# Kernel optimization log

Hardware: AMD Instinct MI355X
Metric: run time of the kernel (lower is better)

The kernel has to match this reference:

```python
import jax, jax.numpy as jnp
import numpy as np

R = 16
ALPHA = 32
SCALING = ALPHA / R  # 2.0


def setup_inputs() -> dict:
    key = jax.random.key(0)
    k1, k2, k3, k4, k5 = jax.random.split(key, 5)
    x = jax.random.normal(k1, (8192, 4096), dtype=jnp.float32)
    W = jax.random.normal(k2, (4096, 4096), dtype=jnp.float32) * 0.02
    b = jax.random.normal(k3, (4096,), dtype=jnp.float32) * 0.02
    A = jax.random.uniform(k4, (R, 4096), dtype=jnp.float32)
    B = jax.random.normal(k5, (4096, R), dtype=jnp.float32) * 0.02
    return {"x": x, "W": W, "b": b, "A": A, "B": B}


def reference(x, W, b, A, B):
    # base linear: x @ W.T + b
    base = jnp.einsum("ni,oi->no", x, W) + b
    # LoRA path, reassociated: scaling * ((x @ A.T) @ B.T)
    # mathematically identical to x @ (scaling * (B @ A)).T but O(r*(in+out)) per token
    lora = SCALING * jnp.einsum("nr,or->no", jnp.einsum("ni,ri->nr", x, A), B)
    return base + lora
```

## Files before the change

kernel.cpp:

```cpp
#include <hip/hip_runtime.h>
#include <stdint.h>

typedef unsigned short u16;
typedef __bf16 bf16x8 __attribute__((ext_vector_type(8)));
typedef u16   u16x8  __attribute__((ext_vector_type(8)));
typedef float f32x4  __attribute__((ext_vector_type(4)));
typedef float f32x16 __attribute__((ext_vector_type(16)));

#define GLOBAL_AS __attribute__((address_space(1)))
#define LDS_AS __attribute__((address_space(3)))

#define MDIM 8192
#define NDIM 4096
#define KDIM 4096
#define RDIM 16

#define BM 128
#define BN 128
#define BK 64
#define EXTS 40

#define XBF_OFF 0
#define WBF_OFF (MDIM * KDIM * 2)
#define ABF_OFF (WBF_OFF + NDIM * KDIM * 2)
#define T_OFF   (ABF_OFF + RDIM * KDIM * 2)
#define WS_NEED ((size_t)T_OFF + MDIM * RDIM * 4)

#define XN8 (MDIM * KDIM / 8)
#define WN8 (NDIM * KDIM / 8)
#define AN8 (RDIM * KDIM / 8)

__device__ __forceinline__ u16 f2bf(float f) {
    union { float f; uint32_t u; } un;
    un.f = f;
    uint32_t u = un.u;
    u += 0x7FFFu + ((u >> 16) & 1u);
    return (u16)(u >> 16);
}

__device__ __forceinline__ void cvt8(const float* __restrict__ p, u16* __restrict__ d) {
    f32x4 a = *(const f32x4*)p;
    f32x4 b = *(const f32x4*)(p + 4);
    u16x8 o;
    o[0] = f2bf(a[0]); o[1] = f2bf(a[1]); o[2] = f2bf(a[2]); o[3] = f2bf(a[3]);
    o[4] = f2bf(b[0]); o[5] = f2bf(b[1]); o[6] = f2bf(b[2]); o[7] = f2bf(b[3]);
    *(u16x8*)d = o;
}

__global__ __launch_bounds__(256) void cvt_all_kernel(
        const float* __restrict__ x, const float* __restrict__ W,
        const float* __restrict__ A,
        u16* __restrict__ xbf, u16* __restrict__ Wbf, u16* __restrict__ Abf) {
    const int total = XN8 + WN8 + AN8;
    int i = blockIdx.x * blockDim.x + threadIdx.x;
    const int stride = gridDim.x * blockDim.x;
    for (; i < total; i += stride) {
        if (i < XN8) {
            cvt8(x + (size_t)i * 8, xbf + (size_t)i * 8);
        } else if (i < XN8 + WN8) {
            const int j = i - XN8;
            cvt8(W + (size_t)j * 8, Wbf + (size_t)j * 8);
        } else {
            const int j = i - XN8 - WN8;
            cvt8(A + (size_t)j * 8, Abf + (size_t)j * 8);
        }
    }
}

__global__ __launch_bounds__(256) void lora_t_kernel(
        const u16* __restrict__ x, const u16* __restrict__ A,
        float* __restrict__ t) {
    const int wave = threadIdx.x >> 6;
    const int lane = threadIdx.x & 63;
    const int rl   = lane & 15;
    const int quad = lane >> 4;
    const int m0   = (blockIdx.x * 4 + wave) * 16;

    const u16* xp = x + (size_t)(m0 + rl) * KDIM + quad * 8;
    const u16* ap = A + (size_t)rl * KDIM + quad * 8;

    f32x4 acc = {0.f, 0.f, 0.f, 0.f};
#pragma unroll 8
    for (int k = 0; k < KDIM; k += 32) {
        bf16x8 av = *(const bf16x8*)(xp + k);
        bf16x8 bv = *(const bf16x8*)(ap + k);
        acc = __builtin_amdgcn_mfma_f32_16x16x32_bf16(av, bv, acc, 0, 0, 0);
    }
    const int orow = m0 + quad * 4;
#pragma unroll
    for (int v = 0; v < 4; ++v)
        t[(size_t)(orow + v) * RDIM + rl] = acc[v];
}

__global__ __launch_bounds__(256) void lora_t_inline_kernel(
        const float* __restrict__ x, const float* __restrict__ A,
        float* __restrict__ t) {
    const int wave = threadIdx.x >> 6;
    const int lane = threadIdx.x & 63;
    const int rl   = lane & 15;
    const int quad = lane >> 4;
    const int m0   = (blockIdx.x * 4 + wave) * 16;

    const float* xp = x + (size_t)(m0 + rl) * KDIM + quad * 8;
    const float* ap = A + (size_t)rl * KDIM + quad * 8;

    f32x4 acc = {0.f, 0.f, 0.f, 0.f};
    for (int k = 0; k < KDIM; k += 32) {
        f32x4 a0 = *(const f32x4*)(xp + k), a1 = *(const f32x4*)(xp + k + 4);
        f32x4 b0 = *(const f32x4*)(ap + k), b1 = *(const f32x4*)(ap + k + 4);
        u16x8 av, bv;
#pragma unroll
        for (int j = 0; j < 4; ++j) {
            av[j] = f2bf(a0[j]); av[j + 4] = f2bf(a1[j]);
            bv[j] = f2bf(b0[j]); bv[j + 4] = f2bf(b1[j]);
        }
        acc = __builtin_amdgcn_mfma_f32_16x16x32_bf16(
            (bf16x8)av, (bf16x8)bv, acc, 0, 0, 0);
    }
    const int orow = m0 + quad * 4;
#pragma unroll
    for (int v = 0; v < 4; ++v)
        t[(size_t)(orow + v) * RDIM + rl] = acc[v];
}

#define BK2   64
#define HTILE 8192
#define ABUF  16384
#define BOFFS 32768
#define NKT   (KDIM / BK2)

#define STAGE(gsrc, half, kt, par, ab) do {                                   \
    const int _b = (par) * ABUF + (ab) * BOFFS + (half) * HTILE;              \
    _Pragma("unroll")                                                         \
    for (int _q = 0; _q < 2; ++_q) {                                          \
        const int _c   = _q * 512 + tid;                                      \
        const int _row = _c >> 3;                                             \
        const int _kc  = (_c & 7) ^ (_row & 7);                               \
        __builtin_amdgcn_global_load_lds(                                     \
            (const GLOBAL_AS uint32_t*)((gsrc) +                              \
                (size_t)((half) * 128 + _row) * KDIM + (kt) * BK2 + _kc * 8), \
            (LDS_AS uint32_t*)(smem + _b + _c * 8), 16, 0, 0);                \
    } } while (0)

#define NOSTAGE ((void)0)
#define VM0 asm volatile("s_waitcnt vmcnt(0)" ::: "memory")

#define READ_A32(dst, ab_, c) do {                                            \
    _Pragma("unroll")                                                         \
    for (int h = 0; h < 2; ++h)                                               \
        _Pragma("unroll")                                                     \
        for (int r = 0; r < 2; ++r) {                                         \
            const int rh = wm * 64 + r * 32 + l31;                            \
            dst[h][r] = *(const bf16x8*)((ab_) + h * HTILE + rh * 64 +        \
                                         ((((c) * 2 + hi) ^ (rh & 7)) * 8));  \
        } } while (0)

#define READ_B32(dst, bb_, c) do {                                            \
    _Pragma("unroll")                                                         \
    for (int cb = 0; cb < 2; ++cb) {                                          \
        const int rh = wn * 32 + l31;                                         \
        dst[cb] = *(const bf16x8*)((bb_) + cb * HTILE + rh * 64 +             \
                                   ((((c) * 2 + hi) ^ (rh & 7)) * 8));        \
    } } while (0)

#define MFMA32(a_, b_) do {                                                   \
    __builtin_amdgcn_s_setprio(1);                                            \
    _Pragma("unroll")                                                         \
    for (int h = 0; h < 2; ++h)                                               \
        _Pragma("unroll")                                                     \
        for (int r = 0; r < 2; ++r)                                           \
            _Pragma("unroll")                                                 \
            for (int cb = 0; cb < 2; ++cb)                                    \
                acc[h][r][cb] = __builtin_amdgcn_mfma_f32_32x32x16_bf16(      \
                    a_[h][r], b_[cb], acc[h][r][cb], 0, 0, 0);                \
    __builtin_amdgcn_s_setprio(0);                                            \
} while (0)

#define BARRIER __builtin_amdgcn_s_barrier()

#define KT32(ab_, bb_, S1, S2, S3, S4, WEND) do {                             \
    READ_A32(aF, ab_, 0); READ_B32(bF, bb_, 0);                               \
    S1; S2;                                                                   \
    READ_A32(aN, ab_, 1); READ_B32(bN, bb_, 1);                               \
    MFMA32(aF, bF);                                                           \
    S3;                                                                       \
    READ_A32(aF, ab_, 2); READ_B32(bF, bb_, 2);                               \
    MFMA32(aN, bN);                                                           \
    S4;                                                                       \
    READ_A32(aN, ab_, 3); READ_B32(bN, bb_, 3);                               \
    MFMA32(aF, bF);                                                           \
    MFMA32(aN, bN);                                                           \
    WEND; BARRIER;                                                            \
} while (0)

__global__ __launch_bounds__(512, 2) void gemm8_lora_kernel(
        const u16* __restrict__ x, const u16* __restrict__ W,
        const float* __restrict__ bias, const float* __restrict__ Bl,
        const float* __restrict__ tmat, float* __restrict__ out) {
    __shared__ __align__(16) u16 smem[65536];

    const int tid  = threadIdx.x;
    const int lane = tid & 63;
    const int wave = tid >> 6;
    const int wm   = wave >> 2;
    const int wn   = wave & 3;
    const int l31  = lane & 31;
    const int hi   = lane >> 5;
    const int bm   = blockIdx.y * 256;
    const int bn   = blockIdx.x * 256;

    const u16* gA = x + (size_t)bm * KDIM;
    const u16* gB = W + (size_t)bn * KDIM;

    f32x16 acc[2][2][2];
#pragma unroll
    for (int h = 0; h < 2; ++h)
#pragma unroll
        for (int r = 0; r < 2; ++r)
#pragma unroll
            for (int cb = 0; cb < 2; ++cb)
                acc[h][r][cb] = (f32x16)(0.f);

    bf16x8 aF[2][2], aN[2][2], bF[2], bN[2];

    STAGE(gA, 0, 0, 0, 0); STAGE(gA, 1, 0, 0, 0);
    STAGE(gB, 0, 0, 0, 1); STAGE(gB, 1, 0, 0, 1);
    VM0;
    BARRIER;

    for (int t = 0; t < NKT - 1; ++t) {
        const u16* ab = smem + (t & 1) * ABUF;
        const u16* bb = smem + BOFFS + (t & 1) * ABUF;
        const int par = (t & 1) ^ 1;
        KT32(ab, bb,
             STAGE(gA, 0, t + 1, par, 0), STAGE(gA, 1, t + 1, par, 0),
             STAGE(gB, 0, t + 1, par, 1), STAGE(gB, 1, t + 1, par, 1),
             VM0);
    }
    {
        const u16* ab = smem + ABUF;
        const u16* bb = smem + BOFFS + ABUF;
        KT32(ab, bb, NOSTAGE, NOSTAGE, NOSTAGE, NOSTAGE, NOSTAGE);
    }

    if (tid < 256) {
        const float* tp = tmat + (size_t)(bm + tid) * RDIM;
        u16* d = smem + tid * 16;
        f32x4 t0 = *(const f32x4*)tp,       t1 = *(const f32x4*)(tp + 4);
        f32x4 t2 = *(const f32x4*)(tp + 8), t3 = *(const f32x4*)(tp + 12);
        u16x8 o0, o1;
#pragma unroll
        for (int j = 0; j < 4; ++j) {
            o0[j] = f2bf(2.0f * t0[j]); o0[j + 4] = f2bf(2.0f * t1[j]);
            o1[j] = f2bf(2.0f * t2[j]); o1[j + 4] = f2bf(2.0f * t3[j]);
        }
        *(u16x8*)d = o0; *(u16x8*)(d + 8) = o1;
    } else {
        const int r = tid - 256;
        const float* bp = Bl + (size_t)(bn + r) * RDIM;
        u16* d = smem + 4096 + r * 16;
        f32x4 b0 = *(const f32x4*)bp,       b1 = *(const f32x4*)(bp + 4);
        f32x4 b2 = *(const f32x4*)(bp + 8), b3 = *(const f32x4*)(bp + 12);
        u16x8 o0, o1;
#pragma unroll
        for (int j = 0; j < 4; ++j) {
            o0[j] = f2bf(b0[j]); o0[j + 4] = f2bf(b1[j]);
            o1[j] = f2bf(b2[j]); o1[j + 4] = f2bf(b3[j]);
        }
        *(u16x8*)d = o0; *(u16x8*)(d + 8) = o1;
    }
    __syncthreads();

    {
        bf16x8 ae[2][2], be[2];
#pragma unroll
        for (int h = 0; h < 2; ++h)
#pragma unroll
            for (int r = 0; r < 2; ++r) {
                const int row = h * 128 + wm * 64 + r * 32 + l31;
                ae[h][r] = *(const bf16x8*)(smem + row * 16 + hi * 8);
            }
#pragma unroll
        for (int cb = 0; cb < 2; ++cb) {
            const int row = cb * 128 + wn * 32 + l31;
            be[cb] = *(const bf16x8*)(smem + 4096 + row * 16 + hi * 8);
        }
#pragma unroll
        for (int h = 0; h < 2; ++h)
#pragma unroll
            for (int r = 0; r < 2; ++r)
#pragma unroll
                for (int cb = 0; cb < 2; ++cb)
                    acc[h][r][cb] = __builtin_amdgcn_mfma_f32_32x32x16_bf16(
                        ae[h][r], be[cb], acc[h][r][cb], 0, 0, 0);
    }

    float bv[2];
#pragma unroll
    for (int cb = 0; cb < 2; ++cb)
        bv[cb] = bias[bn + cb * 128 + wn * 32 + l31];
#pragma unroll
    for (int h = 0; h < 2; ++h)
#pragma unroll
        for (int r = 0; r < 2; ++r) {
            const int row0 = bm + h * 128 + wm * 64 + r * 32 + 4 * hi;
#pragma unroll
            for (int cb = 0; cb < 2; ++cb) {
                const int gcol = bn + cb * 128 + wn * 32 + l31;
#pragma unroll
                for (int reg = 0; reg < 16; ++reg) {
                    const int grow = row0 + (reg & 3) + 8 * (reg >> 2);
                    out[(size_t)grow * NDIM + gcol] = acc[h][r][cb][reg] + bv[cb];
                }
            }
        }
}

__device__ __forceinline__ void stage_ext_b(
        int tid, int bm, int bn,
        const float* __restrict__ t, const float* __restrict__ bias,
        const float* __restrict__ Bl, u16* eA, u16* eB) {
    if (tid < 128) {
        const int r = tid;
        const float* tp = t + (size_t)(bm + r) * RDIM;
        u16* d = eA + r * EXTS;
#pragma unroll
        for (int j = 0; j < RDIM; ++j) d[j] = f2bf(2.0f * tp[j]);
        d[16] = 0x3F80;
#pragma unroll
        for (int j = 17; j < 32; ++j) d[j] = 0;
    } else {
        const int r = tid - 128;
        const float* bp = Bl + (size_t)(bn + r) * RDIM;
        u16* d = eB + r * EXTS;
#pragma unroll
        for (int j = 0; j < RDIM; ++j) d[j] = f2bf(bp[j]);
        d[16] = f2bf(bias[bn + r]);
#pragma unroll
        for (int j = 17; j < 32; ++j) d[j] = 0;
    }
}

__global__ __launch_bounds__(256) void gemm_lora_inline_kernel(
        const float* __restrict__ x, const float* __restrict__ W,
        const float* __restrict__ bias, const float* __restrict__ Bl,
        const float* __restrict__ t, float* __restrict__ out) {
    __shared__ __align__(16) u16 sA[BM * BK];
    __shared__ __align__(16) u16 sB[BN * BK];
    __shared__ __align__(16) u16 sAe[BM * EXTS];
    __shared__ __align__(16) u16 sBe[BN * EXTS];

    const int tid  = threadIdx.x;
    const int lane = tid & 63;
    const int wave = tid >> 6;
    const int wm   = wave >> 1;
    const int wn   = wave & 1;
    const int rl   = lane & 15;
    const int quad = lane >> 4;
    const int bm   = blockIdx.y * BM;
    const int bn   = blockIdx.x * BN;

    stage_ext_b(tid, bm, bn, t, bias, Bl, sAe, sBe);

    const float* gA = x + (size_t)bm * KDIM;
    const float* gB = W + (size_t)bn * KDIM;

    const int row0 = tid >> 3;
    const int kc0  = tid & 7;

    f32x4 acc[4][4];
#pragma unroll
    for (int i = 0; i < 4; ++i)
#pragma unroll
        for (int j = 0; j < 4; ++j)
            acc[i][j] = (f32x4){0.f, 0.f, 0.f, 0.f};

    for (int kt = 0; kt < KDIM; kt += BK) {
        u16x8 ra[4], rb[4];
#pragma unroll
        for (int q = 0; q < 4; ++q) {
            const int row = q * 32 + row0;
            const int kc  = kc0 ^ (row & 7);
            const size_t base = (size_t)row * KDIM + kt + kc * 8;
            f32x4 a0 = *(const f32x4*)(gA + base), a1 = *(const f32x4*)(gA + base + 4);
            f32x4 b0 = *(const f32x4*)(gB + base), b1 = *(const f32x4*)(gB + base + 4);
#pragma unroll
            for (int j = 0; j < 4; ++j) {
                ra[q][j] = f2bf(a0[j]); ra[q][j + 4] = f2bf(a1[j]);
                rb[q][j] = f2bf(b0[j]); rb[q][j + 4] = f2bf(b1[j]);
            }
        }
        __syncthreads();
#pragma unroll
        for (int q = 0; q < 4; ++q) {
            const int c = q * 256 + tid;
            *(u16x8*)(sA + c * 8) = ra[q];
            *(u16x8*)(sB + c * 8) = rb[q];
        }
        __syncthreads();

#pragma unroll
        for (int kk = 0; kk < 2; ++kk) {
            const int lc = kk * 4 + quad;
            bf16x8 af[4], bfv[4];
#pragma unroll
            for (int i = 0; i < 4; ++i) {
                const int rra = wm * 64 + i * 16 + rl;
                const int rrb = wn * 64 + i * 16 + rl;
                af[i]  = *(const bf16x8*)(sA + rra * BK + (lc ^ (rra & 7)) * 8);
                bfv[i] = *(const bf16x8*)(sB + rrb * BK + (lc ^ (rrb & 7)) * 8);
            }
#pragma unroll
            for (int i = 0; i < 4; ++i)
#pragma unroll
                for (int j = 0; j < 4; ++j)
                    acc[i][j] = __builtin_amdgcn_mfma_f32_16x16x32_bf16(
                        af[i], bfv[j], acc[i][j], 0, 0, 0);
        }
    }

    {
        const int ko = quad * 8;
        bf16x8 af[4], bfv[4];
#pragma unroll
        for (int i = 0; i < 4; ++i) {
            af[i]  = *(const bf16x8*)(sAe + (wm * 64 + i * 16 + rl) * EXTS + ko);
            bfv[i] = *(const bf16x8*)(sBe + (wn * 64 + i * 16 + rl) * EXTS + ko);
        }
#pragma unroll
        for (int i = 0; i < 4; ++i)
#pragma unroll
            for (int j = 0; j < 4; ++j)
                acc[i][j] = __builtin_amdgcn_mfma_f32_16x16x32_bf16(
                    af[i], bfv[j], acc[i][j], 0, 0, 0);
    }

#pragma unroll
    for (int i = 0; i < 4; ++i) {
        const int grow = bm + wm * 64 + i * 16 + quad * 4;
#pragma unroll
        for (int j = 0; j < 4; ++j) {
            const int gcol = bn + wn * 64 + j * 16 + rl;
#pragma unroll
            for (int v = 0; v < 4; ++v)
                out[(size_t)(grow + v) * NDIM + gcol] = acc[i][j][v];
        }
    }
}

extern "C" void kernel_launch(void* const* d_in, const int* in_sizes, int n_in,
                              void* d_out, int out_size, void* d_ws, size_t ws_size,
                              hipStream_t stream) {
    const float* x  = (const float*)d_in[0];
    const float* W  = (const float*)d_in[1];
    const float* b  = (const float*)d_in[2];
    const float* A  = (const float*)d_in[3];
    const float* Bl = (const float*)d_in[4];
    float* out = (float*)d_out;
    char* ws = (char*)d_ws;

    if (ws_size >= WS_NEED) {
        u16*   xbf = (u16*)(ws + XBF_OFF);
        u16*   Wbf = (u16*)(ws + WBF_OFF);
        u16*   Abf = (u16*)(ws + ABF_OFF);
        float* t   = (float*)(ws + T_OFF);

        dim3 grid8(NDIM / 256, MDIM / 256);
        cvt_all_kernel<<<4096, 256, 0, stream>>>(x, W, A, xbf, Wbf, Abf);
        lora_t_kernel<<<128, 256, 0, stream>>>(xbf, Abf, t);
        gemm8_lora_kernel<<<grid8, 512, 0, stream>>>(xbf, Wbf, b, Bl, t, out);
    } else {
        float* t = (float*)ws;
        dim3 grid(NDIM / BN, MDIM / BM);
        lora_t_inline_kernel<<<128, 256, 0, stream>>>(x, A, t);
        gemm_lora_inline_kernel<<<grid, 256, 0, stream>>>(x, W, b, Bl, t, out);
    }
}
```

Before: 566.5 us.

## Use 16-wave blocks with 64x64 wave tiles and XCD-aware block remap

Grows the GEMM block from 512 to 1024 threads. Each wave now owns a 64x64 output sub-tile instead of 128x64, which halves the accumulator registers and doubles resident waves per CU. It also remaps the block index so consecutive blocks on the same XCD share nearby output tiles for L2 reuse. The hand-interleaved fragment prefetch is replaced by a simpler per-chunk load-then-MFMA loop, which raises LDS reads per MFMA and may expose LDS latency.

After: 571.8 us. Within noise of the previous version (+0.9%).

```diff
diff --git a/kernel.cpp b/kernel.cpp
--- a/kernel.cpp
+++ b/kernel.cpp
@@ -130,70 +130,19 @@
 #define NKT   (KDIM / BK2)
 
 #define STAGE(gsrc, half, kt, par, ab) do {                                   \
-    const int _b = (par) * ABUF + (ab) * BOFFS + (half) * HTILE;              \
-    _Pragma("unroll")                                                         \
-    for (int _q = 0; _q < 2; ++_q) {                                          \
-        const int _c   = _q * 512 + tid;                                      \
-        const int _row = _c >> 3;                                             \
-        const int _kc  = (_c & 7) ^ (_row & 7);                               \
-        __builtin_amdgcn_global_load_lds(                                     \
-            (const GLOBAL_AS uint32_t*)((gsrc) +                              \
-                (size_t)((half) * 128 + _row) * KDIM + (kt) * BK2 + _kc * 8), \
-            (LDS_AS uint32_t*)(smem + _b + _c * 8), 16, 0, 0);                \
-    } } while (0)
-
-#define NOSTAGE ((void)0)
+    const int _row = tid >> 3;                                                \
+    const int _kc  = (tid & 7) ^ (_row & 7);                                  \
+    __builtin_amdgcn_global_load_lds(                                         \
+        (const GLOBAL_AS uint32_t*)((gsrc) +                                  \
+            (size_t)((half) * 128 + _row) * KDIM + (kt) * BK2 + _kc * 8),     \
+        (LDS_AS uint32_t*)(smem + (par) * ABUF + (ab) * BOFFS +               \
+                           (half) * HTILE + tid * 8), 16, 0, 0);              \
+} while (0)
+
 #define VM0 asm volatile("s_waitcnt vmcnt(0)" ::: "memory")
-
-#define READ_A32(dst, ab_, c) do {                                            \
-    _Pragma("unroll")                                                         \
-    for (int h = 0; h < 2; ++h)                                               \
-        _Pragma("unroll")                                                     \
-        for (int r = 0; r < 2; ++r) {                                         \
-            const int rh = wm * 64 + r * 32 + l31;                            \
-            dst[h][r] = *(const bf16x8*)((ab_) + h * HTILE + rh * 64 +        \
-                                         ((((c) * 2 + hi) ^ (rh & 7)) * 8));  \
-        } } while (0)
-
-#define READ_B32(dst, bb_, c) do {                                            \
-    _Pragma("unroll")                                                         \
-    for (int cb = 0; cb < 2; ++cb) {                                          \
-        const int rh = wn * 32 + l31;                                         \
-        dst[cb] = *(const bf16x8*)((bb_) + cb * HTILE + rh * 64 +             \
-                                   ((((c) * 2 + hi) ^ (rh & 7)) * 8));        \
-    } } while (0)
-
-#define MFMA32(a_, b_) do {                                                   \
-    __builtin_amdgcn_s_setprio(1);                                            \
-    _Pragma("unroll")                                                         \
-    for (int h = 0; h < 2; ++h)                                               \
-        _Pragma("unroll")                                                     \
-        for (int r = 0; r < 2; ++r)                                           \
-            _Pragma("unroll")                                                 \
-            for (int cb = 0; cb < 2; ++cb)                                    \
-                acc[h][r][cb] = __builtin_amdgcn_mfma_f32_32x32x16_bf16(      \
-                    a_[h][r], b_[cb], acc[h][r][cb], 0, 0, 0);                \
-    __builtin_amdgcn_s_setprio(0);                                            \
-} while (0)
-
 #define BARRIER __builtin_amdgcn_s_barrier()
 
-#define KT32(ab_, bb_, S1, S2, S3, S4, WEND) do {                             \
-    READ_A32(aF, ab_, 0); READ_B32(bF, bb_, 0);                               \
-    S1; S2;                                                                   \
-    READ_A32(aN, ab_, 1); READ_B32(bN, bb_, 1);                               \
-    MFMA32(aF, bF);                                                           \
-    S3;                                                                       \
-    READ_A32(aF, ab_, 2); READ_B32(bF, bb_, 2);                               \
-    MFMA32(aN, bN);                                                           \
-    S4;                                                                       \
-    READ_A32(aN, ab_, 3); READ_B32(bN, bb_, 3);                               \
-    MFMA32(aF, bF);                                                           \
-    MFMA32(aN, bN);                                                           \
-    WEND; BARRIER;                                                            \
-} while (0)
-
-__global__ __launch_bounds__(512, 2) void gemm8_lora_kernel(
+__global__ __launch_bounds__(1024) void gemm8_lora_kernel(
         const u16* __restrict__ x, const u16* __restrict__ W,
         const float* __restrict__ bias, const float* __restrict__ Bl,
         const float* __restrict__ tmat, float* __restrict__ out) {
@@ -206,41 +155,66 @@
     const int wn   = wave & 3;
     const int l31  = lane & 31;
     const int hi   = lane >> 5;
-    const int bm   = blockIdx.y * 256;
-    const int bn   = blockIdx.x * 256;
+    const int s7   = l31 & 7;
+
+    const int lid  = blockIdx.y * gridDim.x + blockIdx.x;
+    const int nlid = (lid & 7) * 64 + (lid >> 3);
+    const int bm   = (nlid >> 4) * 256;
+    const int bn   = (nlid & 15) * 256;
 
     const u16* gA = x + (size_t)bm * KDIM;
     const u16* gB = W + (size_t)bn * KDIM;
 
-    f32x16 acc[2][2][2];
-#pragma unroll
-    for (int h = 0; h < 2; ++h)
-#pragma unroll
-        for (int r = 0; r < 2; ++r)
-#pragma unroll
-            for (int cb = 0; cb < 2; ++cb)
-                acc[h][r][cb] = (f32x16)(0.f);
-
-    bf16x8 aF[2][2], aN[2][2], bF[2], bN[2];
+    int aoff[2], boff[2];
+#pragma unroll
+    for (int r = 0; r < 2; ++r) {
+        const int ra = wm * 64 + r * 32 + l31;
+        aoff[r] = (ra >> 7) * HTILE + (ra & 127) * 64;
+        const int rb = wn * 64 + r * 32 + l31;
+        boff[r] = (rb >> 7) * HTILE + (rb & 127) * 64;
+    }
+
+    f32x16 acc[2][2];
+#pragma unroll
+    for (int r = 0; r < 2; ++r)
+#pragma unroll
+        for (int cb = 0; cb < 2; ++cb)
+            acc[r][cb] = (f32x16)(0.f);
 
     STAGE(gA, 0, 0, 0, 0); STAGE(gA, 1, 0, 0, 0);
     STAGE(gB, 0, 0, 0, 1); STAGE(gB, 1, 0, 0, 1);
     VM0;
     BARRIER;
 
-    for (int t = 0; t < NKT - 1; ++t) {
+    for (int t = 0; t < NKT; ++t) {
         const u16* ab = smem + (t & 1) * ABUF;
         const u16* bb = smem + BOFFS + (t & 1) * ABUF;
-        const int par = (t & 1) ^ 1;
-        KT32(ab, bb,
-             STAGE(gA, 0, t + 1, par, 0), STAGE(gA, 1, t + 1, par, 0),
-             STAGE(gB, 0, t + 1, par, 1), STAGE(gB, 1, t + 1, par, 1),
-             VM0);
-    }
-    {
-        const u16* ab = smem + ABUF;
-        const u16* bb = smem + BOFFS + ABUF;
-        KT32(ab, bb, NOSTAGE, NOSTAGE, NOSTAGE, NOSTAGE, NOSTAGE);
+        const bool more = (t < NKT - 1);
+        if (more) {
+            const int par = (t & 1) ^ 1;
+            STAGE(gA, 0, t + 1, par, 0); STAGE(gA, 1, t + 1, par, 0);
+            STAGE(gB, 0, t + 1, par, 1); STAGE(gB, 1, t + 1, par, 1);
+        }
+#pragma unroll
+        for (int c = 0; c < 4; ++c) {
+            const int ko = (((c * 2 + hi) ^ s7) * 8);
+            bf16x8 af[2], bfr[2];
+#pragma unroll
+            for (int r = 0; r < 2; ++r) {
+                af[r]  = *(const bf16x8*)(ab + aoff[r] + ko);
+                bfr[r] = *(const bf16x8*)(bb + boff[r] + ko);
+            }
+            __builtin_amdgcn_s_setprio(1);
+#pragma unroll
+            for (int r = 0; r < 2; ++r)
+#pragma unroll
+                for (int cb = 0; cb < 2; ++cb)
+                    acc[r][cb] = __builtin_amdgcn_mfma_f32_32x32x16_bf16(
+                        af[r], bfr[cb], acc[r][cb], 0, 0, 0);
+            __builtin_amdgcn_s_setprio(0);
+        }
+        if (more) VM0;
+        BARRIER;
     }
 
     if (tid < 256) {
@@ -255,7 +229,7 @@
             o1[j] = f2bf(2.0f * t2[j]); o1[j + 4] = f2bf(2.0f * t3[j]);
         }
         *(u16x8*)d = o0; *(u16x8*)(d + 8) = o1;
-    } else {
+    } else if (tid < 512) {
         const int r = tid - 256;
         const float* bp = Bl + (size_t)(bn + r) * RDIM;
         u16* d = smem + 4096 + r * 16;
@@ -272,48 +246,39 @@
     __syncthreads();
 
     {
-        bf16x8 ae[2][2], be[2];
-#pragma unroll
-        for (int h = 0; h < 2; ++h)
-#pragma unroll
-            for (int r = 0; r < 2; ++r) {
-                const int row = h * 128 + wm * 64 + r * 32 + l31;
-                ae[h][r] = *(const bf16x8*)(smem + row * 16 + hi * 8);
+        bf16x8 ae[2], be[2];
+#pragma unroll
+        for (int r = 0; r < 2; ++r) {
+            const int ra = wm * 64 + r * 32 + l31;
+            ae[r] = *(const bf16x8*)(smem + ra * 16 + hi * 8);
+            const int rb = wn * 64 + r * 32 + l31;
+            be[r] = *(const bf16x8*)(smem + 4096 + rb * 16 + hi * 8);
+        }
+#pragma unroll
+        for (int r = 0; r < 2; ++r)
+#pragma unroll
+            for (int cb = 0; cb < 2; ++cb)
+                acc[r][cb] = __builtin_amdgcn_mfma_f32_32x32x16_bf16(
+                    ae[r], be[cb], acc[r][cb], 0, 0, 0);
+    }
+
+    float bv[2];
+#pragma unroll
+    for (int cb = 0; cb < 2; ++cb)
+        bv[cb] = bias[bn + wn * 64 + cb * 32 + l31];
+#pragma unroll
+    for (int r = 0; r < 2; ++r) {
+        const int row0 = bm + wm * 64 + r * 32 + 4 * hi;
+#pragma unroll
+        for (int cb = 0; cb < 2; ++cb) {
+            const int gcol = bn + wn * 64 + cb * 32 + l31;
+#pragma unroll
+            for (int reg = 0; reg < 16; ++reg) {
+                const int grow = row0 + (reg & 3) + 8 * (reg >> 2);
+                out[(size_t)grow * NDIM + gcol] = acc[r][cb][reg] + bv[cb];
             }
-#pragma unroll
-        for (int cb = 0; cb < 2; ++cb) {
-            const int row = cb * 128 + wn * 32 + l31;
-            be[cb] = *(const bf16x8*)(smem + 4096 + row * 16 + hi * 8);
-        }
-#pragma unroll
-        for (int h = 0; h < 2; ++h)
-#pragma unroll
-            for (int r = 0; r < 2; ++r)
-#pragma unroll
-                for (int cb = 0; cb < 2; ++cb)
-                    acc[h][r][cb] = __builtin_amdgcn_mfma_f32_32x32x16_bf16(
-                        ae[h][r], be[cb], acc[h][r][cb], 0, 0, 0);
-    }
-
-    float bv[2];
-#pragma unroll
-    for (int cb = 0; cb < 2; ++cb)
-        bv[cb] = bias[bn + cb * 128 + wn * 32 + l31];
-#pragma unroll
-    for (int h = 0; h < 2; ++h)
-#pragma unroll
-        for (int r = 0; r < 2; ++r) {
-            const int row0 = bm + h * 128 + wm * 64 + r * 32 + 4 * hi;
-#pragma unroll
-            for (int cb = 0; cb < 2; ++cb) {
-                const int gcol = bn + cb * 128 + wn * 32 + l31;
-#pragma unroll
-                for (int reg = 0; reg < 16; ++reg) {
-                    const int grow = row0 + (reg & 3) + 8 * (reg >> 2);
-                    out[(size_t)grow * NDIM + gcol] = acc[h][r][cb][reg] + bv[cb];
-                }
-            }
-        }
+        }
+    }
 }
 
 __device__ __forceinline__ void stage_ext_b(
@@ -468,7 +433,7 @@
         dim3 grid8(NDIM / 256, MDIM / 256);
         cvt_all_kernel<<<4096, 256, 0, stream>>>(x, W, A, xbf, Wbf, Abf);
         lora_t_kernel<<<128, 256, 0, stream>>>(xbf, Abf, t);
-        gemm8_lora_kernel<<<grid8, 512, 0, stream>>>(xbf, Wbf, b, Bl, t, out);
+        gemm8_lora_kernel<<<grid8, 1024, 0, stream>>>(xbf, Wbf, b, Bl, t, out);
     } else {
         float* t = (float*)ws;
         dim3 grid(NDIM / BN, MDIM / BM);
```
